# Performance work log

Measured on AMD Instinct MI355X. Metric: run time of the kernel, lower is better.

The kernel has to match this reference:

```python
import jax, jax.numpy as jnp
import numpy as np

N_NODES = 100000
N_EDGES = 3200000
D_FEAT = 128


def setup_inputs() -> dict:
    key = jax.random.key(0)
    k1, k2, k3 = jax.random.split(key, 3)
    edges = jax.random.randint(k1, (2, N_EDGES), 0, N_NODES, dtype=jnp.int64)
    attentions = jax.random.uniform(k2, (N_EDGES,), dtype=jnp.float32)
    X = jax.random.normal(k3, (N_NODES, D_FEAT), dtype=jnp.float32)
    return {"edges": edges, "attentions": attentions, "N": N_NODES, "X": X}


def reference(edges, attentions, N, X):
    # Sparse COO adjacency (rows=edges[0], cols=edges[1], vals=attentions)
    # times dense X: out[i] = sum over edges (i -> j) of att_e * X[j]
    src = edges[0]  # row index i
    dst = edges[1]  # col index j
    messages = attentions[:, None] * X[dst]          # [E, D] gather + weight
    out = jax.ops.segment_sum(messages, src, num_segments=N)  # [N, D] scatter-add
    return out
```

## Files before the change

kernel.cpp:

```cpp
#include <hip/hip_runtime.h>

typedef unsigned int u32;
typedef unsigned short u16;


constexpr int D_FEAT  = 128;
constexpr int N_NODES = 100000;
constexpr int BROWS   = 128;
constexpr int KB      = (N_NODES + BROWS - 1) / BROWS;
constexpr int EPT     = 12;
constexpr int CHUNK   = 1024 * EPT;
constexpr int NCONV   = 192;
constexpr int CAP     = 4608;
constexpr int RPT     = CAP / 512;
constexpr int NPAN    = 8;
constexpr int NCELL   = NPAN * BROWS;
constexpr int SPILL_CAP = 65536;

__device__ __forceinline__ u32 rne_bf16(float f) {
    u32 u = __float_as_uint(f);
    return (u + 0x7FFFu + ((u >> 16) & 1u)) >> 16;
}

__device__ __forceinline__ u32 pack_rec(int s, int d, float a) {
    u32 q = (u32)(a * 255.0f + 0.5f);
    return ((u32)(s & 127) << 25) | ((u32)d << 8) | q;
}

__device__ __forceinline__ u32 cell_of(u32 rec) {
    return (((rec >> 22) & 7u) << 7) | (rec >> 25);
}

__global__ __launch_bounds__(1024) void scatter_fused(
    const int* __restrict__ src, const int* __restrict__ dst,
    const float* __restrict__ att, u32* __restrict__ gcur,
    int2* __restrict__ spill, u32* __restrict__ epack,
    const float* __restrict__ X, uint2* __restrict__ Xb,
    int E, int nconv)
{
    const int blk = blockIdx.x;
    if (blk < nconv) {
        const int nthreads = nconv * 1024;
        const float4* __restrict__ X4 = (const float4*)X;
        for (int u = blk * 1024 + threadIdx.x; u < N_NODES * 32; u += nthreads) {
            float4 v = X4[u];
            uint2 o;
            o.x = rne_bf16(v.x) | (rne_bf16(v.y) << 16);
            o.y = rne_bf16(v.z) | (rne_bf16(v.w) << 16);
            Xb[u] = o;
        }
        return;
    }

    __shared__ u32 lcnt[KB], lbase[KB];
    const int c  = blk - nconv;
    const int e0 = c * CHUNK;
    const int e1 = min(e0 + CHUNK, E);
    const int tid = threadIdx.x;

    for (int i = tid; i < KB; i += 1024) lcnt[i] = 0;
    __syncthreads();

    u32 rec[EPT]; int rb[EPT];
    #pragma unroll
    for (int k = 0; k < EPT; ++k) rb[k] = -1;
    const int base = e0 + tid * EPT;
    const bool v4ok = ((E & 3) == 0);
    if (v4ok && base + EPT <= e1) {
        #pragma unroll
        for (int q4 = 0; q4 < EPT / 4; ++q4) {
            int4   sv = *(const int4*)(src + base + q4 * 4);
            int4   dv = *(const int4*)(dst + base + q4 * 4);
            float4 av = *(const float4*)(att + base + q4 * 4);
            #pragma unroll
            for (int k = 0; k < 4; ++k) {
                const int idx = q4 * 4 + k;
                const int s = (&sv.x)[k];
                rb[idx]  = s >> 7;
                rec[idx] = pack_rec(s, (&dv.x)[k], (&av.x)[k]);
                atomicAdd(&lcnt[rb[idx]], 1u);
            }
        }
    } else {
        #pragma unroll
        for (int k = 0; k < EPT; ++k) {
            int i = base + k;
            if (i < e1) {
                int s = src[i];
                rb[k] = s >> 7;
                rec[k] = pack_rec(s, dst[i], att[i]);
                atomicAdd(&lcnt[rb[k]], 1u);
            }
        }
    }
    __syncthreads();

    const int rot = (c * 131) % KB;
    for (int i = tid; i < KB; i += 1024) {
        int j = i + rot; if (j >= KB) j -= KB;
        u32 cc = lcnt[j];
        lbase[j] = cc ? atomicAdd(&gcur[j], cc) : 0u;
        lcnt[j] = 0;
    }
    __syncthreads();

    #pragma unroll
    for (int k = 0; k < EPT; ++k) {
        if (rb[k] >= 0) {
            u32 pos = lbase[rb[k]] + atomicAdd(&lcnt[rb[k]], 1u);
            if (pos < (u32)CAP) {
                epack[(size_t)rb[k] * CAP + pos] = rec[k];
            } else {
                u32 sp = atomicAdd(&gcur[KB], 1u);
                if (sp < (u32)SPILL_CAP) {
                    int d = (int)((rec[k] >> 8) & 0x1FFFFu);
                    int q = (int)(rec[k] & 255u);
                    int s = (rb[k] << 7) | (int)(rec[k] >> 25);
                    spill[sp] = make_int2(s, (d << 8) | q);
                }
            }
        }
    }
}

__global__ __launch_bounds__(512) void accumulate_bucket_bf16(
    const u32* __restrict__ gcur, const u32* __restrict__ epack,
    const uint2* __restrict__ Xb, float* __restrict__ out, int N)
{
    __shared__ u32 ebuf[CAP];
    __shared__ u32 cnt[NCELL], off[NCELL], cur[NCELL];
    const int b   = blockIdx.x;
    const int tid = threadIdx.x;
    const int g   = tid >> 5;
    const int l   = tid & 31;
    const u32 s  = (u32)b * CAP;
    const int nb = min((int)gcur[b], CAP);
    const int row0 = b * BROWS;
    const int rows = min(BROWS, N - row0);

    u32 rec[RPT];
    #pragma unroll
    for (int k = 0; k < RPT; ++k) {
        int i = tid + k * 512;
        rec[k] = (i < nb) ? epack[s + i] : 0u;
    }
    for (int i = tid; i < NCELL; i += 512) cnt[i] = 0;
    __syncthreads();
    #pragma unroll
    for (int k = 0; k < RPT; ++k)
        if (tid + k * 512 < nb) atomicAdd(&cnt[cell_of(rec[k])], 1u);
    __syncthreads();
    if (tid < 64) {
        u32 c[16]; u32 tot = 0;
        #pragma unroll
        for (int k = 0; k < 16; ++k) { c[k] = cnt[tid * 16 + k]; tot += c[k]; }
        u32 incl = tot;
        #pragma unroll
        for (int o = 1; o < 64; o <<= 1) {
            u32 v = __shfl_up(incl, o, 64);
            if (tid >= o) incl += v;
        }
        u32 run = incl - tot;
        #pragma unroll
        for (int k = 0; k < 16; ++k) {
            off[tid * 16 + k] = run; cur[tid * 16 + k] = run; run += c[k];
        }
    }
    __syncthreads();
    #pragma unroll
    for (int k = 0; k < RPT; ++k)
        if (tid + k * 512 < nb) {
            u32 pos = atomicAdd(&cur[cell_of(rec[k])], 1u);
            ebuf[pos] = rec[k] & 0x01FFFFFFu;
        }
    __syncthreads();

    float4 acc[8];
    #pragma unroll
    for (int ri = 0; ri < 8; ++ri) acc[ri] = make_float4(0.f, 0.f, 0.f, 0.f);

    for (int p = 0; p < NPAN; ++p) {
        #pragma unroll
        for (int ri = 0; ri < 8; ++ri) {
            const int r = (ri << 4) + g;
            const u32 cell = ((u32)p << 7) | (u32)r;
            const u32 base = off[cell];
            const u32 n    = cnt[cell];
            float4 a4 = acc[ri];
            u32 j = 0;
            for (; j + 2 <= n; j += 2) {
                const u32 p0 = ebuf[base + j];
                const u32 p1 = ebuf[base + j + 1];
                const uint2 q0 = Xb[(size_t)(p0 >> 8) * 32 + l];
                const uint2 q1 = Xb[(size_t)(p1 >> 8) * 32 + l];
                const float a0 = (float)(p0 & 255u) * (1.0f / 255.0f);
                const float a1 = (float)(p1 & 255u) * (1.0f / 255.0f);
                a4.x = fmaf(a0, __uint_as_float(q0.x << 16),         a4.x);
                a4.y = fmaf(a0, __uint_as_float(q0.x & 0xFFFF0000u), a4.y);
                a4.z = fmaf(a0, __uint_as_float(q0.y << 16),         a4.z);
                a4.w = fmaf(a0, __uint_as_float(q0.y & 0xFFFF0000u), a4.w);
                a4.x = fmaf(a1, __uint_as_float(q1.x << 16),         a4.x);
                a4.y = fmaf(a1, __uint_as_float(q1.x & 0xFFFF0000u), a4.y);
                a4.z = fmaf(a1, __uint_as_float(q1.y << 16),         a4.z);
                a4.w = fmaf(a1, __uint_as_float(q1.y & 0xFFFF0000u), a4.w);
            }
            if (j < n) {
                const u32 p0 = ebuf[base + j];
                const uint2 q0 = Xb[(size_t)(p0 >> 8) * 32 + l];
                const float a0 = (float)(p0 & 255u) * (1.0f / 255.0f);
                a4.x = fmaf(a0, __uint_as_float(q0.x << 16),         a4.x);
                a4.y = fmaf(a0, __uint_as_float(q0.x & 0xFFFF0000u), a4.y);
                a4.z = fmaf(a0, __uint_as_float(q0.y << 16),         a4.z);
                a4.w = fmaf(a0, __uint_as_float(q0.y & 0xFFFF0000u), a4.w);
            }
            acc[ri] = a4;
        }
    }
    #pragma unroll
    for (int ri = 0; ri < 8; ++ri) {
        const int r = (ri << 4) + g;
        if (r < rows)
            ((float4*)out)[(size_t)(row0 + r) * 32 + l] = acc[ri];
    }
}

__global__ __launch_bounds__(512) void accumulate_bucket_f32(
    const u32* __restrict__ gcur, const u32* __restrict__ epack,
    const float* __restrict__ X, float* __restrict__ out, int N)
{
    __shared__ u32 ebuf[CAP];
    __shared__ u32 cnt[BROWS], off[BROWS], cur[BROWS];
    const int b   = blockIdx.x;
    const int tid = threadIdx.x;
    const int g   = tid >> 5;
    const int l   = tid & 31;
    const u32 s  = (u32)b * CAP;
    const int nb = min((int)gcur[b], CAP);
    const int row0 = b * BROWS;
    const int rows = min(BROWS, N - row0);

    u32 rec[RPT];
    #pragma unroll
    for (int k = 0; k < RPT; ++k) {
        int i = tid + k * 512;
        rec[k] = (i < nb) ? epack[s + i] : 0u;
    }
    if (tid < BROWS) cnt[tid] = 0;
    __syncthreads();
    #pragma unroll
    for (int k = 0; k < RPT; ++k)
        if (tid + k * 512 < nb) atomicAdd(&cnt[rec[k] >> 25], 1u);
    __syncthreads();
    if (tid < 64) {
        u32 c0 = cnt[2 * tid], c1 = cnt[2 * tid + 1];
        u32 ps = c0 + c1;
        u32 incl = ps;
        #pragma unroll
        for (int o = 1; o < 64; o <<= 1) {
            u32 v = __shfl_up(incl, o, 64);
            if (tid >= o) incl += v;
        }
        u32 excl = incl - ps;
        off[2 * tid]     = excl;      cur[2 * tid]     = excl;
        off[2 * tid + 1] = excl + c0; cur[2 * tid + 1] = excl + c0;
    }
    __syncthreads();
    #pragma unroll
    for (int k = 0; k < RPT; ++k)
        if (tid + k * 512 < nb) {
            u32 pos = atomicAdd(&cur[rec[k] >> 25], 1u);
            ebuf[pos] = rec[k] & 0x01FFFFFFu;
        }
    __syncthreads();

    const float4* __restrict__ X4 = (const float4*)X;
    for (int r = g; r < rows; r += 16) {
        const u32 base = off[r];
        const u32 n    = cnt[r];
        float4 acc = make_float4(0.f, 0.f, 0.f, 0.f);
        u32 j = 0;
        for (; j + 4 <= n; j += 4) {
            u32 p[4]; float4 v[4];
            #pragma unroll
            for (int k = 0; k < 4; ++k) p[k] = ebuf[base + j + k];
            #pragma unroll
            for (int k = 0; k < 4; ++k) v[k] = X4[(size_t)(p[k] >> 8) * 32 + l];
            #pragma unroll
            for (int k = 0; k < 4; ++k) {
                const float a = (float)(p[k] & 255u) * (1.0f / 255.0f);
                acc.x = fmaf(a, v[k].x, acc.x); acc.y = fmaf(a, v[k].y, acc.y);
                acc.z = fmaf(a, v[k].z, acc.z); acc.w = fmaf(a, v[k].w, acc.w);
            }
        }
        for (; j < n; ++j) {
            const u32 p = ebuf[base + j];
            const float4 v = X4[(size_t)(p >> 8) * 32 + l];
            const float a = (float)(p & 255u) * (1.0f / 255.0f);
            acc.x = fmaf(a, v.x, acc.x); acc.y = fmaf(a, v.y, acc.y);
            acc.z = fmaf(a, v.z, acc.z); acc.w = fmaf(a, v.w, acc.w);
        }
        ((float4*)out)[(size_t)(row0 + r) * 32 + l] = acc;
    }
}

__global__ __launch_bounds__(256) void spill_fixup(
    const u32* __restrict__ gcur, const int2* __restrict__ spill,
    const float* __restrict__ X, float* __restrict__ out)
{
    const int nspill = min((int)gcur[KB], SPILL_CAP);
    if (nspill == 0) return;
    const int group = (int)((blockIdx.x * blockDim.x + threadIdx.x) >> 5);
    const int lane  = threadIdx.x & 31;
    const int nGroups = (int)((gridDim.x * blockDim.x) >> 5);
    for (int e = group; e < nspill; e += nGroups) {
        const int2 p = spill[e];
        const int s = p.x, d = p.y >> 8;
        const float a = (float)(p.y & 255) * (1.0f / 255.0f);
        const float4 v = ((const float4*)(X + (size_t)d * D_FEAT))[lane];
        float* o = out + (size_t)s * D_FEAT + (size_t)lane * 4;
        unsafeAtomicAdd(o + 0, a * v.x);
        unsafeAtomicAdd(o + 1, a * v.y);
        unsafeAtomicAdd(o + 2, a * v.z);
        unsafeAtomicAdd(o + 3, a * v.w);
    }
}

__global__ __launch_bounds__(256) void spmm_edge_atomic(
    const int* __restrict__ src, const int* __restrict__ dst,
    const float* __restrict__ att, const float* __restrict__ X,
    float* __restrict__ out, int E)
{
    const int group = (int)((blockIdx.x * blockDim.x + threadIdx.x) >> 5);
    const int lane  = threadIdx.x & 31;
    const int nGroups = (int)((gridDim.x * blockDim.x) >> 5);
    for (int e = group; e < E; e += nGroups) {
        const int s = src[e], d = dst[e];
        const float a = att[e];
        const float4 v = ((const float4*)(X + (size_t)d * D_FEAT))[lane];
        float* o = out + (size_t)s * D_FEAT + (size_t)lane * 4;
        unsafeAtomicAdd(o + 0, a * v.x);
        unsafeAtomicAdd(o + 1, a * v.y);
        unsafeAtomicAdd(o + 2, a * v.z);
        unsafeAtomicAdd(o + 3, a * v.w);
    }
}

static inline size_t align16(size_t x) { return (x + 15) & ~(size_t)15; }

extern "C" void kernel_launch(void* const* d_in, const int* in_sizes, int n_in,
                              void* d_out, int out_size, void* d_ws, size_t ws_size,
                              hipStream_t stream) {
    const int*   edges = (const int*)d_in[0];
    const float* att   = (const float*)d_in[1];
    const float* X     = (const float*)d_in[3];
    float*       out   = (float*)d_out;

    const int E = in_sizes[1];
    const int N = N_NODES;
    const int* src = edges;
    const int* dst = edges + E;
    const int nchunk = (E + CHUNK - 1) / CHUNK;

    size_t o_gcur  = 0;
    size_t o_spill = align16(o_gcur + ((size_t)KB + 1) * 4);
    size_t o_epack = align16(o_spill + (size_t)SPILL_CAP * 8);
    size_t o_xb    = align16(o_epack + (size_t)KB * CAP * 4);
    size_t need_f32  = o_xb;
    size_t need_bf16 = o_xb + (size_t)N * D_FEAT * 2;

    if (ws_size < need_f32) {
        hipMemsetAsync(d_out, 0, (size_t)out_size * sizeof(float), stream);
        const int grid = (E + 7) / 8;
        spmm_edge_atomic<<<grid, 256, 0, stream>>>(src, dst, att, X, out, E);
        return;
    }

    char* ws = (char*)d_ws;
    u32*  gcur  = (u32*)(ws + o_gcur);
    int2* spill = (int2*)(ws + o_spill);
    u32*  epack = (u32*)(ws + o_epack);
    uint2* Xb   = (uint2*)(ws + o_xb);

    const bool use_bf16 = (ws_size >= need_bf16);
    const int nconv = use_bf16 ? NCONV : 0;

    hipMemsetAsync(gcur, 0, ((size_t)KB + 1) * 4, stream);

    scatter_fused<<<nconv + nchunk, 1024, 0, stream>>>(
        src, dst, att, gcur, spill, epack, X, Xb, E, nconv);

    if (use_bf16)
        accumulate_bucket_bf16<<<KB, 512, 0, stream>>>(gcur, epack, Xb, out, N);
    else
        accumulate_bucket_f32<<<KB, 512, 0, stream>>>(gcur, epack, X, out, N);

    spill_fixup<<<128, 256, 0, stream>>>(gcur, spill, X, out);
}
```

Before: 250.6 us.

## Stage bucketed edge records in shared memory before coalesced global scatter

The binning kernel now computes a block-wide prefix sum over per-bucket counts, writes each edge record into a locally sorted shared-memory buffer, then has consecutive threads copy runs into the global bucket arrays, finding the bucket by binary search. This makes the global stores to epack mostly contiguous per bucket instead of scattered single-word writes. In exchange it adds a 10-step scan with many barriers, a binary search per record, and about 48KB more shared memory, which can lower occupancy. It also drops the rotated ordering of the global atomics and assumes KB is at most 1024.

```diff
diff --git a/kernel.cpp b/kernel.cpp
--- a/kernel.cpp
+++ b/kernel.cpp
@@ -52,13 +52,18 @@
         return;
     }
 
-    __shared__ u32 lcnt[KB], lbase[KB];
+    __shared__ u32 sbuf[CHUNK];
+    __shared__ u32 lcnt[KB];
+    __shared__ u32 lbase[KB];
+    __shared__ u32 loff[KB + 1];
+    __shared__ u32 ssc[1024];
     const int c  = blk - nconv;
     const int e0 = c * CHUNK;
     const int e1 = min(e0 + CHUNK, E);
+    const int n  = e1 - e0;
     const int tid = threadIdx.x;
 
-    for (int i = tid; i < KB; i += 1024) lcnt[i] = 0;
+    if (tid < KB) lcnt[tid] = 0;
     __syncthreads();
 
     u32 rec[EPT]; int rb[EPT];
@@ -95,29 +100,48 @@
     }
     __syncthreads();
 
-    const int rot = (c * 131) % KB;
-    for (int i = tid; i < KB; i += 1024) {
-        int j = i + rot; if (j >= KB) j -= KB;
-        u32 cc = lcnt[j];
-        lbase[j] = cc ? atomicAdd(&gcur[j], cc) : 0u;
-        lcnt[j] = 0;
-    }
-    __syncthreads();
-
-    #pragma unroll
-    for (int k = 0; k < EPT; ++k) {
+    u32 tot = (tid < KB) ? lcnt[tid] : 0u;
+    ssc[tid] = tot;
+    __syncthreads();
+    for (int o = 1; o < 1024; o <<= 1) {
+        u32 v = (tid >= o) ? ssc[tid - o] : 0u;
+        __syncthreads();
+        ssc[tid] += v;
+        __syncthreads();
+    }
+    if (tid < KB) {
+        loff[tid]  = ssc[tid] - tot;
+        lbase[tid] = tot ? atomicAdd(&gcur[tid], tot) : 0u;
+        lcnt[tid]  = 0;
+    }
+    if (tid == 1023) loff[KB] = ssc[1023];
+    __syncthreads();
+
+    #pragma unroll
+    for (int k = 0; k < EPT; ++k)
         if (rb[k] >= 0) {
-            u32 pos = lbase[rb[k]] + atomicAdd(&lcnt[rb[k]], 1u);
-            if (pos < (u32)CAP) {
-                epack[(size_t)rb[k] * CAP + pos] = rec[k];
-            } else {
-                u32 sp = atomicAdd(&gcur[KB], 1u);
-                if (sp < (u32)SPILL_CAP) {
-                    int d = (int)((rec[k] >> 8) & 0x1FFFFu);
-                    int q = (int)(rec[k] & 255u);
-                    int s = (rb[k] << 7) | (int)(rec[k] >> 25);
-                    spill[sp] = make_int2(s, (d << 8) | q);
-                }
+            u32 pos = loff[rb[k]] + atomicAdd(&lcnt[rb[k]], 1u);
+            sbuf[pos] = rec[k];
+        }
+    __syncthreads();
+
+    for (int i = tid; i < n; i += 1024) {
+        int lo = 0, hi = KB;
+        while (hi - lo > 1) {
+            int mid = (lo + hi) >> 1;
+            if (loff[mid] <= (u32)i) lo = mid; else hi = mid;
+        }
+        u32 r = sbuf[i];
+        u32 pos = lbase[lo] + ((u32)i - loff[lo]);
+        if (pos < (u32)CAP) {
+            epack[(size_t)lo * CAP + pos] = r;
+        } else {
+            u32 sp = atomicAdd(&gcur[KB], 1u);
+            if (sp < (u32)SPILL_CAP) {
+                int d = (int)((r >> 8) & 0x1FFFFu);
+                int q = (int)(r & 255u);
+                int s = (lo << 7) | (int)(r >> 25);
+                spill[sp] = make_int2(s, (d << 8) | q);
             }
         }
     }
```

Measured after the change: 241.0 us (median of 2 runs). -3.8%, faster.
